# Performance work log

Measured on AMD Instinct MI355X. Metric: run time of the kernel, lower is better.

The kernel has to match this reference:

```python
import jax, jax.numpy as jnp
import numpy as np

B, T, F, H = 64, 512, 1024, 1024

def setup_inputs() -> dict:
    key = jax.random.key(0)
    ks = jax.random.split(key, 13)
    def w(k, shape):
        return jax.random.normal(k, shape, dtype=jnp.float32) * 0.02
    inp = {"x": jax.random.normal(ks[0], (B, T, F), dtype=jnp.float32)}
    names = ["i", "f", "g", "o"]
    for j, n in enumerate(names):
        inp[f"U_{n}"] = w(ks[1 + 3 * j], (F, H))
        inp[f"V_{n}"] = w(ks[2 + 3 * j], (H, H))
        inp[f"b_{n}"] = w(ks[3 + 3 * j], (H,))
    return inp


def reference(x, U_i, V_i, b_i, U_f, V_f, b_f, U_g, V_g, b_g, U_o, V_o, b_o):
    batch = x.shape[0]
    hid = V_i.shape[0]
    # Concatenate the 4 gate projections into single GEMMs (same math, fused).
    U = jnp.concatenate([U_i, U_f, U_g, U_o], axis=1)  # [F, 4H]
    V = jnp.concatenate([V_i, V_f, V_g, V_o], axis=1)  # [H, 4H]
    b = jnp.concatenate([b_i, b_f, b_g, b_o], axis=0)  # [4H]
    # Precompute input contribution for all timesteps in one big GEMM.
    xU = jnp.einsum("btf,fk->btk", x, U) + b           # [B, T, 4H]
    xU_t = jnp.swapaxes(xU, 0, 1)                       # [T, B, 4H]

    def step(carry, xu):
        h, c = carry
        z = xu + h @ V                                  # [B, 4H]
        zi, zf, zg, zo = jnp.split(z, 4, axis=-1)
        i_t = jax.nn.sigmoid(zi)
        f_t = jax.nn.sigmoid(zf)
        g_t = jnp.tanh(zg)
        o_t = jnp.tanh(zo)  # NOTE: source uses tanh (not sigmoid) for output gate
        c = f_t * c + i_t * g_t
        h = o_t * jnp.tanh(c)
        return (h, c), None

    h0 = jnp.zeros((batch, hid), dtype=x.dtype)
    c0 = jnp.zeros((batch, hid), dtype=x.dtype)
    (h_t, c_t), _ = jax.lax.scan(step, (h0, c0), xU_t)
    return h_t
```

## Files before the change

kernel.cpp:

```cpp
#include <hip/hip_runtime.h>
#include <hip/hip_cooperative_groups.h>

using u16 = unsigned short;
using u32 = unsigned int;
using u64 = unsigned long long;
using bf16x8 = __attribute__((ext_vector_type(8))) short;
using f16x8  = __attribute__((ext_vector_type(8))) _Float16;
using f32x4  = __attribute__((ext_vector_type(4))) float;
using u32x4  = __attribute__((ext_vector_type(4))) unsigned int;

static constexpr size_t XU_OFF = 0;
static constexpr size_t XU_BYTES = (size_t)512 * 64 * 4096 * 2;
static constexpr size_t XB_OFF = XU_OFF + XU_BYTES;
static constexpr size_t XB_BYTES = (size_t)64 * 512 * 1024 * 2;
static constexpr size_t UT_OFF = XB_OFF + XB_BYTES;
static constexpr size_t WT_BYTES = (size_t)4096 * 1024 * 2;
static constexpr size_t VT_OFF = UT_OFF + WT_BYTES;
static constexpr size_t BP_OFF = VT_OFF + WT_BYTES;
static constexpr size_t BP_BYTES = 4096 * 4;
static constexpr size_t HT_PLANE = (size_t)2 * 4 * 16 * 1024 * 2;
static constexpr size_t HHI_OFF = BP_OFF + BP_BYTES;
static constexpr size_t FLAG_OFF = HHI_OFF + HT_PLANE;

__device__ __forceinline__ float bf2f(u32 u) {
    return __uint_as_float(u << 16);
}
__device__ __forceinline__ u16 f2bf(float f) {
    u32 u = __float_as_uint(f);
    u32 r = (u + 0x7FFFu + ((u >> 16) & 1u)) >> 16;
    return (u16)r;
}
__device__ __forceinline__ u16 f2h(float f) {
    _Float16 x = (_Float16)f;
    union { _Float16 h; u16 u; } cv;
    cv.h = x;
    return cv.u;
}

__device__ __forceinline__ float fast_sigmoid(float x) {
    return __builtin_amdgcn_rcpf(1.f + __expf(-x));
}
__device__ __forceinline__ float fast_tanh(float x) {
    return 1.f - 2.f * __builtin_amdgcn_rcpf(1.f + __expf(2.f * x));
}

__device__ __forceinline__ u32x4 load16_uc(const u16* p) {
    u32x4 v;
    asm volatile("global_load_dwordx4 %0, %1, off sc0 sc1"
                 : "=v"(v)
                 : "v"(p));
    return v;
}

__device__ __forceinline__ void store16_wt(u16* p, u32x4 v) {
    asm volatile("global_store_dwordx4 %0, %1, off sc0 sc1 nt"
                 :: "v"(p), "v"(v) : "memory");
}

__device__ __forceinline__ void wait_vm4(int j, u32x4& a) {
    switch (j) {
    case 0:  asm volatile("s_waitcnt vmcnt(3)" : "+v"(a)); break;
    case 1:  asm volatile("s_waitcnt vmcnt(2)" : "+v"(a)); break;
    case 2:  asm volatile("s_waitcnt vmcnt(1)" : "+v"(a)); break;
    default: asm volatile("s_waitcnt vmcnt(0)" : "+v"(a)); break;
    }
}

__device__ __forceinline__ void gld16(const u16* g, u16* l) {
    __builtin_amdgcn_global_load_lds((const __attribute__((address_space(1))) void*)g,
                                     (__attribute__((address_space(3))) void*)l,
                                     16, 0, 0);
}

__device__ __forceinline__ void wait_chunk(const u32* cnt, int c) {
    for (;;) {
        u32 v = __hip_atomic_load(cnt + c, __ATOMIC_RELAXED, __HIP_MEMORY_SCOPE_AGENT);
        if (v >= 2048u) break;
        __builtin_amdgcn_s_sleep(8);
    }
    asm volatile("" ::: "memory");
}

__device__ __forceinline__ void gemm_tile(int tau,
        const u16* __restrict__ xb, const u16* __restrict__ UT,
        const float* __restrict__ bp, u16* __restrict__ xu,
        u16* As, u16* Bs, u16* Cs, u32* cnt) {
    int tc = tau >> 11, rem = tau & 2047;
    int b = rem >> 5, nt = rem & 31, mt = b * 4 + tc;
    int tid = threadIdx.x;
    int lane = tid & 63, wv = tid >> 6;
    int wm = wv >> 2, wn = wv & 3;
    int l15 = lane & 15, quad = lane >> 4;

    int idr = tid >> 2, idk = (tid & 3) * 8;
    const u16* aS = xb + (size_t)(mt * 128 + idr) * 1024 + idk;
    const u16* bS = UT + (size_t)(nt * 128 + idr) * 1024 + idk;
    u16* aD = As + (size_t)tid * 8;
    u16* bD = Bs + (size_t)tid * 8;

    f32x4 acc[4][2];
#pragma unroll
    for (int i = 0; i < 4; ++i)
#pragma unroll
        for (int j = 0; j < 2; ++j) acc[i][j] = f32x4{0.f, 0.f, 0.f, 0.f};

    float biasv[2];
#pragma unroll
    for (int j = 0; j < 2; ++j) biasv[j] = bp[nt * 128 + wn * 32 + j * 16 + l15];

    for (int k0 = 0; k0 < 1024; k0 += 32) {
        gld16(aS + k0, aD);
        gld16(bS + k0, bD);
        __syncthreads();
        bf16x8 af[4], bfv[2];
#pragma unroll
        for (int i = 0; i < 4; ++i)
            af[i] = *(const bf16x8*)(As + (size_t)(wm * 64 + i * 16 + l15) * 32 + quad * 8);
#pragma unroll
        for (int j = 0; j < 2; ++j)
            bfv[j] = *(const bf16x8*)(Bs + (size_t)(wn * 32 + j * 16 + l15) * 32 + quad * 8);
#pragma unroll
        for (int i = 0; i < 4; ++i)
#pragma unroll
            for (int j = 0; j < 2; ++j)
                acc[i][j] = __builtin_amdgcn_mfma_f32_16x16x32_bf16(af[i], bfv[j], acc[i][j], 0, 0, 0);
        __syncthreads();
    }

#pragma unroll
    for (int i = 0; i < 4; ++i)
#pragma unroll
        for (int j = 0; j < 2; ++j)
#pragma unroll
            for (int rg = 0; rg < 4; ++rg)
                Cs[(size_t)(wm * 64 + i * 16 + quad * 4 + rg) * 136 + wn * 32 + j * 16 + l15] =
                    f2bf(acc[i][j][rg] + biasv[j]);
    __syncthreads();

#pragma unroll
    for (int p = 0; p < 4; ++p) {
        int id = p * 512 + tid;
        int row = id >> 4, q = id & 15;
        u32x4 v = *(const u32x4*)(Cs + (size_t)row * 136 + q * 8);
        int gr = mt * 128 + row;
        int t_i = gr & 511, b_i = gr >> 9;
        store16_wt(xu + (((size_t)(t_i * 64 + b_i)) << 12) + nt * 128 + q * 8, v);
    }
    asm volatile("s_waitcnt vmcnt(0)" ::: "memory");
    __syncthreads();
    if (tid == 0)
        __hip_atomic_fetch_add(cnt + tc, 1u, __ATOMIC_RELAXED, __HIP_MEMORY_SCOPE_AGENT);
}

__global__ void __launch_bounds__(512, 2) lstm_fused_kernel(
        const float* __restrict__ x,
        const float* U0, const float* V0, const float* b0,
        const float* U1, const float* V1, const float* b1,
        const float* U2, const float* V2, const float* b2,
        const float* U3, const float* V3, const float* b3,
        char* __restrict__ ws, float* __restrict__ out) {
    __shared__ u16 As[128 * 32];
    __shared__ u16 Bs[128 * 32];
    __shared__ u16 Cs[128 * 136];
    __shared__ float zs[8][16][132];

    u16*   xb  = (u16*)(ws + XB_OFF);
    u16*   UT  = (u16*)(ws + UT_OFF);
    u16*   VT  = (u16*)(ws + VT_OFF);
    float* bp  = (float*)(ws + BP_OFF);
    u16*   xu  = (u16*)(ws + XU_OFF);
    u16*   hhi = (u16*)(ws + HHI_OFF);
    u32*   flags = (u32*)(ws + FLAG_OFF);
    u32*   cnt   = (u32*)(ws + FLAG_OFF + 2048);

    int bx = blockIdx.x;
    int tid = threadIdx.x;

    if (bx == 0) {
        __hip_atomic_store(flags + tid, 0u, __ATOMIC_RELAXED, __HIP_MEMORY_SCOPE_AGENT);
        __hip_atomic_store(flags + 512 + tid, 0u, __ATOMIC_RELAXED, __HIP_MEMORY_SCOPE_AGENT);
    }
    if (bx == 1) {
        const float* bsrc[4] = {b0, b1, b2, b3};
#pragma unroll
        for (int it = 0; it < 8; ++it) {
            int n = it * 512 + tid;
            bp[n] = bsrc[n & 3][n >> 2];
        }
    }
    {
        const float4* x4 = (const float4*)x;
        uint2* xb4 = (uint2*)xb;
        int t0 = bx * 512 + tid;
#pragma unroll 4
        for (int k = 0; k < 64; ++k) {
            int idx = t0 + k * 131072;
            float4 v = x4[idx];
            uint2 o;
            o.x = (u32)f2bf(v.x) | ((u32)f2bf(v.y) << 16);
            o.y = (u32)f2bf(v.z) | ((u32)f2bf(v.w) << 16);
            xb4[idx] = o;
        }
    }
    {
        u16* tile = Cs;
        const float* srcs[8] = {U0, U1, U2, U3, V0, V1, V2, V3};
        for (int vb = 0; vb < 8; ++vb) {
            int vbx = bx * 8 + vb;
            int mat = vbx >> 8, rem = vbx & 255;
            int tf = rem >> 4, th = rem & 15;
            int f0 = tf * 64, h0 = th * 64;
            const float* s = srcs[mat];
            u16* d = (mat < 4) ? UT : VT;
            bool isU = (mat < 4);
            int gg = mat & 3;
            if (tid < 256) {
                int cc = tid & 63, rr = tid >> 6;
#pragma unroll
                for (int i = 0; i < 16; ++i) {
                    int fr = rr + i * 4;
                    float v = s[(size_t)(f0 + fr) * 1024 + h0 + cc];
                    tile[fr * 65 + cc] = isU ? f2bf(v) : f2h(v);
                }
            }
            __syncthreads();
            if (tid < 256) {
                int cc = tid & 63, rr = tid >> 6;
#pragma unroll
                for (int i = 0; i < 16; ++i) {
                    int hcl = rr + i * 4;
                    d[(size_t)((h0 + hcl) * 4 + gg) * 1024 + f0 + cc] = tile[cc * 65 + hcl];
                }
            }
            __syncthreads();
        }
    }
    __threadfence();
    cooperative_groups::this_grid().sync();

    for (int p = 0; p < 8; ++p)
        gemm_tile(bx * 8 + p, xb, UT, bp, xu, As, Bs, Cs, cnt);

    if (bx >= 128) {
        int gid = bx - 128;
        for (int p = 0; p < 48; ++p)
            gemm_tile(2048 + p * 128 + gid, xb, UT, bp, xu, As, Bs, Cs, cnt);
        return;
    }

    int g  = bx & 3;
    int cb = bx >> 2;
    int lane = tid & 63, wv = tid >> 6;
    int l15 = lane & 15, quad = lane >> 4;
    int r  = tid >> 5;
    int hc = tid & 31;

    f16x8 vfrag[8][4];
    {
        const u16* vb = VT + ((size_t)(cb * 128 + l15) * 1024) + wv * 128 + quad * 8;
#pragma unroll
        for (int nt = 0; nt < 8; ++nt)
#pragma unroll
            for (int j = 0; j < 4; ++j)
                vfrag[nt][j] = *(const f16x8*)(vb + (size_t)nt * 16 * 1024 + j * 32);
    }

    u32* gflags = flags + g * 64;
    int myp = 4 * wv + (lane & 3);

    float c = 0.f;
    float h = 0.f;

    wait_chunk(cnt, 0);
    uint2 xraw = *(const uint2*)(xu + ((size_t)(g * 16 + r) << 12) + cb * 128 + hc * 4);

    for (int t = 0; t < 512; ++t) {
        f32x4 acc[8];
#pragma unroll
        for (int nt = 0; nt < 8; ++nt) acc[nt] = f32x4{0.f, 0.f, 0.f, 0.f};

        if (t) {
            for (;;) {
                u32 f = __hip_atomic_load(gflags + myp, __ATOMIC_RELAXED,
                                          __HIP_MEMORY_SCOPE_AGENT);
                if (__ballot(f >= (u32)t) == ~0ull) break;
                __builtin_amdgcn_s_sleep(1);
            }
            asm volatile("" ::: "memory");

            const u16* hB = hhi + (((size_t)(t & 1) * 4 + g) * 16 + l15) * 1024
                          + wv * 128 + quad * 8;
            u32x4 hv[4];
#pragma unroll
            for (int j = 0; j < 4; ++j)
                hv[j] = load16_uc(hB + j * 32);
#pragma unroll
            for (int j = 0; j < 4; ++j) {
                wait_vm4(j, hv[j]);
                union { u32x4 q; f16x8 v; } ah;
                ah.q = hv[j];
#pragma unroll
                for (int nt = 0; nt < 8; ++nt)
                    acc[nt] = __builtin_amdgcn_mfma_f32_16x16x32_f16(ah.v, vfrag[nt][j], acc[nt], 0, 0, 0);
            }
        }

#pragma unroll
        for (int nt = 0; nt < 8; ++nt)
#pragma unroll
            for (int rg = 0; rg < 4; ++rg)
                zs[wv][quad * 4 + rg][nt * 16 + l15] = acc[nt][rg];
        __syncthreads();

        float4 s = {0.f, 0.f, 0.f, 0.f};
#pragma unroll
        for (int w = 0; w < 8; ++w) {
            float4 v = *(const float4*)&zs[w][r][hc * 4];
            s.x += v.x; s.y += v.y; s.z += v.z; s.w += v.w;
        }
        float z0 = s.x + bf2f(xraw.x & 0xFFFFu);
        float z1 = s.y + bf2f(xraw.x >> 16);
        float z2 = s.z + bf2f(xraw.y & 0xFFFFu);
        float z3 = s.w + bf2f(xraw.y >> 16);

        float it_ = fast_sigmoid(z0);
        float ft_ = fast_sigmoid(z1);
        float gt_ = fast_tanh(z2);
        float ot_ = fast_tanh(z3);
        c = ft_ * c + it_ * gt_;
        h = ot_ * fast_tanh(c);

        if (t == 511) break;

        size_t sidx = (((size_t)((t + 1) & 1) * 4 + g) * 16 + r) * 1024 + cb * 32 + hc;
        __hip_atomic_store(hhi + sidx, f2h(h), __ATOMIC_RELAXED,
                           __HIP_MEMORY_SCOPE_AGENT);
        asm volatile("s_waitcnt vmcnt(0)" ::: "memory");
        __syncthreads();
        if (tid == 0)
            __hip_atomic_store(gflags + cb, (u32)(t + 1), __ATOMIC_RELAXED,
                               __HIP_MEMORY_SCOPE_AGENT);

        if (((t + 1) & 127) == 0) wait_chunk(cnt, (t + 1) >> 7);
        xraw = *(const uint2*)(xu + ((size_t)((t + 1) * 64 + g * 16 + r) << 12) + cb * 128 + hc * 4);
    }

    out[(size_t)(g * 16 + r) * 1024 + cb * 32 + hc] = h;
}

extern "C" void kernel_launch(void* const* d_in, const int* in_sizes, int n_in,
                              void* d_out, int out_size, void* d_ws, size_t ws_size,
                              hipStream_t stream) {
    char* ws = (char*)d_ws;
    const float* x = (const float*)d_in[0];
    const float *U[4], *V[4], *b[4];
    for (int g = 0; g < 4; ++g) {
        U[g] = (const float*)d_in[1 + 3 * g];
        V[g] = (const float*)d_in[2 + 3 * g];
        b[g] = (const float*)d_in[3 + 3 * g];
    }
    float* out = (float*)d_out;

    void* args[] = {(void*)&x,
                    (void*)&U[0], (void*)&V[0], (void*)&b[0],
                    (void*)&U[1], (void*)&V[1], (void*)&b[1],
                    (void*)&U[2], (void*)&V[2], (void*)&b[2],
                    (void*)&U[3], (void*)&V[3], (void*)&b[3],
                    (void*)&ws, (void*)&out};
    hipLaunchCooperativeKernel((const void*)lstm_fused_kernel, dim3(256), dim3(512),
                               args, 0, stream);
}
```

Before: 2.529 ms.

## Replace chunked GEMM/recurrence overlap with full GEMM then grid sync

Removes the chunked producer/consumer scheme, where 128 blocks began the recurrence while the other blocks kept computing later xU time chunks and signalled them through atomic counters. All blocks now compute 32 GEMM tiles each with plain stores, then a second cooperative grid sync runs before the recurrence starts. This drops the counter polling and the write-through stores, but the recurrence no longer overlaps with most of the input-projection GEMM, which lengthens the critical path.

```diff
diff --git a/kernel.cpp b/kernel.cpp
--- a/kernel.cpp
+++ b/kernel.cpp
@@ -52,11 +52,6 @@
     return v;
 }
 
-__device__ __forceinline__ void store16_wt(u16* p, u32x4 v) {
-    asm volatile("global_store_dwordx4 %0, %1, off sc0 sc1 nt"
-                 :: "v"(p), "v"(v) : "memory");
-}
-
 __device__ __forceinline__ void wait_vm4(int j, u32x4& a) {
     switch (j) {
     case 0:  asm volatile("s_waitcnt vmcnt(3)" : "+v"(a)); break;
@@ -72,21 +67,11 @@
                                      16, 0, 0);
 }
 
-__device__ __forceinline__ void wait_chunk(const u32* cnt, int c) {
-    for (;;) {
-        u32 v = __hip_atomic_load(cnt + c, __ATOMIC_RELAXED, __HIP_MEMORY_SCOPE_AGENT);
-        if (v >= 2048u) break;
-        __builtin_amdgcn_s_sleep(8);
-    }
-    asm volatile("" ::: "memory");
-}
-
 __device__ __forceinline__ void gemm_tile(int tau,
         const u16* __restrict__ xb, const u16* __restrict__ UT,
         const float* __restrict__ bp, u16* __restrict__ xu,
-        u16* As, u16* Bs, u16* Cs, u32* cnt) {
-    int tc = tau >> 11, rem = tau & 2047;
-    int b = rem >> 5, nt = rem & 31, mt = b * 4 + tc;
+        u16* As, u16* Bs, u16* Cs) {
+    int mt = tau >> 5, nt = tau & 31;
     int tid = threadIdx.x;
     int lane = tid & 63, wv = tid >> 6;
     int wm = wv >> 2, wn = wv & 3;
@@ -144,12 +129,9 @@
         u32x4 v = *(const u32x4*)(Cs + (size_t)row * 136 + q * 8);
         int gr = mt * 128 + row;
         int t_i = gr & 511, b_i = gr >> 9;
-        store16_wt(xu + (((size_t)(t_i * 64 + b_i)) << 12) + nt * 128 + q * 8, v);
-    }
-    asm volatile("s_waitcnt vmcnt(0)" ::: "memory");
+        *(u32x4*)(xu + (((size_t)(t_i * 64 + b_i)) << 12) + nt * 128 + q * 8) = v;
+    }
     __syncthreads();
-    if (tid == 0)
-        __hip_atomic_fetch_add(cnt + tc, 1u, __ATOMIC_RELAXED, __HIP_MEMORY_SCOPE_AGENT);
 }
 
 __global__ void __launch_bounds__(512, 2) lstm_fused_kernel(
@@ -171,7 +153,6 @@
     u16*   xu  = (u16*)(ws + XU_OFF);
     u16*   hhi = (u16*)(ws + HHI_OFF);
     u32*   flags = (u32*)(ws + FLAG_OFF);
-    u32*   cnt   = (u32*)(ws + FLAG_OFF + 2048);
 
     int bx = blockIdx.x;
     int tid = threadIdx.x;
@@ -238,15 +219,12 @@
     __threadfence();
     cooperative_groups::this_grid().sync();
 
-    for (int p = 0; p < 8; ++p)
-        gemm_tile(bx * 8 + p, xb, UT, bp, xu, As, Bs, Cs, cnt);
-
-    if (bx >= 128) {
-        int gid = bx - 128;
-        for (int p = 0; p < 48; ++p)
-            gemm_tile(2048 + p * 128 + gid, xb, UT, bp, xu, As, Bs, Cs, cnt);
-        return;
-    }
+    for (int p = 0; p < 32; ++p)
+        gemm_tile(bx * 32 + p, xb, UT, bp, xu, As, Bs, Cs);
+    __threadfence();
+    cooperative_groups::this_grid().sync();
+
+    if (bx >= 128) return;
 
     int g  = bx & 3;
     int cb = bx >> 2;
@@ -271,7 +249,6 @@
     float c = 0.f;
     float h = 0.f;
 
-    wait_chunk(cnt, 0);
     uint2 xraw = *(const uint2*)(xu + ((size_t)(g * 16 + r) << 12) + cb * 128 + hc * 4);
 
     for (int t = 0; t < 512; ++t) {
@@ -341,7 +318,6 @@
             __hip_atomic_store(gflags + cb, (u32)(t + 1), __ATOMIC_RELAXED,
                                __HIP_MEMORY_SCOPE_AGENT);
 
-        if (((t + 1) & 127) == 0) wait_chunk(cnt, (t + 1) >> 7);
         xraw = *(const uint2*)(xu + ((size_t)((t + 1) * 64 + g * 16 + r) << 12) + cb * 128 + hc * 4);
     }
 
```

Result: slower. 2.698 ms (+6.7%).
